# Optimization experiments

Hardware: AMD Instinct MI355X
Metric: run time of the kernel (lower is better)

Reference implementation:

```python
import jax, jax.numpy as jnp
import numpy as np

# Geometry constants matching PointLoss.__init__ defaults
FOV_H = 360.0   # horizontal FOV (deg)
FOV_VU = 3.0    # upper vertical FOV (deg)
DH = 0.5        # delta_h
DV = 0.5        # delta_v
PROJ_H = 52     # int(26 / 0.5)
PROJ_W = 720    # int(360 / 0.5)
THETAC = 0.5    # confidence threshold
LAMDA = 1.0     # fov-loss weight
ANGRATE = 1.0   # anglelossrate
EPS = 1e-8


def setup_inputs() -> dict:
    key = jax.random.key(0)
    ks = jax.random.split(key, 10)
    B, H, W = 64, PROJ_H, PROJ_W
    return {
        "vertexmap_proj": jax.random.normal(ks[0], (B, H, W, 3), jnp.float32),
        "normalmap_proj": jax.random.normal(ks[1], (B, H, W, 3), jnp.float32),
        "uncertainty": jax.random.uniform(ks[2], (B, H, W), jnp.float32),
        "now_normalmap": jax.random.normal(ks[3], (B, H, W, 3), jnp.float32),
        "now_confidencemap": jax.random.uniform(ks[4], (B, H, W), jnp.float32),
        "last_normalmap": jax.random.normal(ks[5], (B, H, W, 3), jnp.float32),
        "last_vertexmap": jax.random.normal(ks[6], (B, H, W, 3), jnp.float32),
        "sx": jnp.zeros((1,), jnp.float32),
        "sq": jnp.zeros((1,), jnp.float32),
        "now_maskmap": jax.random.randint(ks[7], (B, H, W), 0, 2, jnp.int32),
        "last_maskmap": jax.random.randint(ks[8], (B, H, W), 0, 2, jnp.int32),
    }


def _gather_proj(m, flat_idx, B, H, W):
    """Gather pixels of m [B,H,W,(C)] at flat index [B,H,W] -> same shape as m."""
    if m.ndim == 3:
        mf = m.reshape(B, H * W)
        return jnp.take_along_axis(mf, flat_idx.reshape(B, H * W), axis=1).reshape(B, H, W)
    C = m.shape[-1]
    mf = m.reshape(B, H * W, C)
    idx = jnp.broadcast_to(flat_idx.reshape(B, H * W, 1), (B, H * W, C))
    return jnp.take_along_axis(mf, idx, axis=1).reshape(B, H, W, C)


def reference(vertexmap_proj, normalmap_proj, uncertainty, now_normalmap,
              now_confidencemap, last_normalmap, last_vertexmap, sx, sq,
              now_maskmap, last_maskmap):
    B, H, W, _ = vertexmap_proj.shape
    v = vertexmap_proj

    # mask of valid current pixels: maskmap > 0 and normal non-zero
    mask0 = (now_maskmap > 0) & (jnp.sum(jnp.abs(now_normalmap), -1) != 0)

    # spherical re-projection (movegrid=True)
    depth = jnp.sqrt(jnp.sum(v * v, -1) + EPS)
    yaw = jnp.arctan2(v[..., 1], v[..., 0]) * (180.0 / np.pi)
    pitch = jnp.arcsin(jnp.clip(v[..., 2] / depth, -1.0, 1.0)) * (180.0 / np.pi)
    proj_x = (FOV_H / 2 - yaw) / DH
    proj_y = (FOV_VU - pitch) / DV

    # fov loss = masked mse(proj, clamp(proj)) (F.mse_loss default mean)
    m0 = mask0.astype(v.dtype)
    n0 = jnp.maximum(jnp.sum(m0), 1.0)
    fovloss = (jnp.sum(m0 * (proj_x - jnp.clip(proj_x, 0, W - 1)) ** 2)
               + jnp.sum(m0 * (proj_y - jnp.clip(proj_y, 0, H - 1)) ** 2)) / n0

    prx = jnp.round(proj_x)
    pry = jnp.round(proj_y)
    inb = (prx >= 0) & (prx < W) & (pry >= 0) & (pry < H)
    prxi = jnp.clip(prx, 0, W - 1).astype(jnp.int32)
    pryi = jnp.clip(pry, 0, H - 1).astype(jnp.int32)
    flat = pryi * W + prxi  # [B,H,W]

    nl = _gather_proj(last_normalmap, flat, B, H, W)   # last normal at projected pixel
    vl = _gather_proj(last_vertexmap, flat, B, H, W)   # last vertex at projected pixel
    lm = _gather_proj(last_maskmap, flat, B, H, W)

    lastmask = (lm > 0) & (jnp.sum(jnp.abs(nl), -1) != 0)
    mask = mask0 & inb & lastmask & (now_confidencemap >= THETAC)
    m = mask.astype(v.dtype)
    n = jnp.maximum(jnp.sum(m), 1.0)

    # point-to-plane ICP residual, uncertainty-weighted L1
    r = jnp.sum(nl * (v - vl), -1)
    icploss = jnp.sum(m * uncertainty * jnp.abs(r)) / n

    # angular loss: 1 - |cos(angle between normals)|
    nn = normalmap_proj
    cosang = jnp.abs(jnp.sum(nl * nn, -1)) / jnp.sqrt(
        jnp.sum(nl * nl, -1) * jnp.sum(nn * nn, -1) + EPS)
    angloss = jnp.sum(m * uncertainty * (1.0 - cosang)) / n

    sx0, sq0 = sx[0], sq[0]
    total = (jnp.exp(-sx0) * icploss + sx0
             + ANGRATE * jnp.exp(-sq0) * angloss + sq0
             + LAMDA * fovloss)
    return total
```

## Files before the change

### kernel.cpp

```cpp
#include <hip/hip_runtime.h>
#include <math.h>


namespace {
constexpr int B_ = 64, H_ = 52, W_ = 720;
constexpr int HW_ = H_ * W_;
constexpr int NPIX = B_ * HW_;
constexpr int NBLOCKS = 2048;
constexpr int NTHREADS = 256;
constexpr float EPSF = 1e-8f;
constexpr float RAD2DEG = 57.29577951308232f;
}

__global__ __launch_bounds__(NTHREADS) void pointloss_main(
    const float* __restrict__ v,
    const float* __restrict__ nrm,
    const float* __restrict__ unc,
    const float* __restrict__ nown,
    const float* __restrict__ conf,
    const float* __restrict__ lastn,
    const float* __restrict__ lastv,
    const int*   __restrict__ nowm,
    const int*   __restrict__ lastm,
    float* __restrict__ partials)
{
    float s_m0 = 0.f, s_fov = 0.f, s_m = 0.f, s_icp = 0.f, s_ang = 0.f;
    const int stride = NBLOCKS * NTHREADS;
    for (int p = blockIdx.x * NTHREADS + threadIdx.x; p < NPIX; p += stride) {
        const float vx = v[3*p+0], vy = v[3*p+1], vz = v[3*p+2];
        const float ax = nown[3*p+0], ay = nown[3*p+1], az = nown[3*p+2];
        const bool mask0 = (nowm[p] > 0) &&
                           ((fabsf(ax) + fabsf(ay) + fabsf(az)) != 0.0f);

        const float depth = sqrtf(vx*vx + vy*vy + vz*vz + EPSF);
        const float yaw   = atan2f(vy, vx) * RAD2DEG;
        const float pitch = asinf(fminf(fmaxf(vz / depth, -1.f), 1.f)) * RAD2DEG;
        const float px = (180.0f - yaw) * 2.0f;
        const float py = (3.0f - pitch) * 2.0f;

        if (mask0) {
            const float dx = px - fminf(fmaxf(px, 0.f), (float)(W_ - 1));
            const float dy = py - fminf(fmaxf(py, 0.f), (float)(H_ - 1));
            s_m0 += 1.0f;
            s_fov += dx*dx + dy*dy;
        }

        const float prx = rintf(px), pry = rintf(py);
        const bool inb = (prx >= 0.f) && (prx < (float)W_) &&
                         (pry >= 0.f) && (pry < (float)H_);

        if (mask0 && inb && (conf[p] >= 0.5f)) {
            const int gi = (p / HW_) * HW_ + (int)pry * W_ + (int)prx;
            const float lx = lastn[3*gi+0], ly = lastn[3*gi+1], lz = lastn[3*gi+2];
            if ((lastm[gi] > 0) && ((fabsf(lx) + fabsf(ly) + fabsf(lz)) != 0.f)) {
                const float u  = unc[p];
                const float wx = lastv[3*gi+0], wy = lastv[3*gi+1], wz = lastv[3*gi+2];
                const float r  = lx*(vx-wx) + ly*(vy-wy) + lz*(vz-wz);
                const float nx = nrm[3*p+0], ny = nrm[3*p+1], nz = nrm[3*p+2];
                const float dt = lx*nx + ly*ny + lz*nz;
                const float den = (lx*lx + ly*ly + lz*lz) *
                                  (nx*nx + ny*ny + nz*nz) + EPSF;
                const float cosang = fabsf(dt) * rsqrtf(den);
                s_m   += 1.0f;
                s_icp += u * fabsf(r);
                s_ang += u * (1.0f - cosang);
            }
        }
    }

    #pragma unroll
    for (int off = 32; off > 0; off >>= 1) {
        s_m0  += __shfl_down(s_m0,  off);
        s_fov += __shfl_down(s_fov, off);
        s_m   += __shfl_down(s_m,   off);
        s_icp += __shfl_down(s_icp, off);
        s_ang += __shfl_down(s_ang, off);
    }
    __shared__ float red[NTHREADS / 64][5];
    const int lane = threadIdx.x & 63;
    const int wv   = threadIdx.x >> 6;
    if (lane == 0) {
        red[wv][0] = s_m0;  red[wv][1] = s_fov; red[wv][2] = s_m;
        red[wv][3] = s_icp; red[wv][4] = s_ang;
    }
    __syncthreads();
    if (threadIdx.x == 0) {
        float t[5] = {0.f, 0.f, 0.f, 0.f, 0.f};
        for (int w2 = 0; w2 < NTHREADS / 64; ++w2)
            for (int c = 0; c < 5; ++c) t[c] += red[w2][c];
        float* o = partials + blockIdx.x * 5;
        for (int c = 0; c < 5; ++c) o[c] = t[c];
    }
}

__global__ __launch_bounds__(256) void pointloss_finalize(
    const float* __restrict__ partials,
    const float* __restrict__ sx,
    const float* __restrict__ sq,
    float* __restrict__ out)
{
    double a0 = 0, a1 = 0, a2 = 0, a3 = 0, a4 = 0;
    for (int i = threadIdx.x; i < NBLOCKS; i += 256) {
        const float* pp = partials + i * 5;
        a0 += (double)pp[0]; a1 += (double)pp[1]; a2 += (double)pp[2];
        a3 += (double)pp[3]; a4 += (double)pp[4];
    }
    #pragma unroll
    for (int off = 32; off > 0; off >>= 1) {
        a0 += __shfl_down(a0, off);
        a1 += __shfl_down(a1, off);
        a2 += __shfl_down(a2, off);
        a3 += __shfl_down(a3, off);
        a4 += __shfl_down(a4, off);
    }
    __shared__ double red[4][5];
    const int lane = threadIdx.x & 63;
    const int wv   = threadIdx.x >> 6;
    if (lane == 0) {
        red[wv][0] = a0; red[wv][1] = a1; red[wv][2] = a2;
        red[wv][3] = a3; red[wv][4] = a4;
    }
    __syncthreads();
    if (threadIdx.x == 0) {
        double t[5] = {0, 0, 0, 0, 0};
        for (int w2 = 0; w2 < 4; ++w2)
            for (int c = 0; c < 5; ++c) t[c] += red[w2][c];
        const double n0 = fmax(t[0], 1.0);
        const double n  = fmax(t[2], 1.0);
        const double sx0 = (double)sx[0], sq0 = (double)sq[0];
        const double total = exp(-sx0) * (t[3] / n) + sx0
                           + exp(-sq0) * (t[4] / n) + sq0
                           + t[1] / n0;
        out[0] = (float)total;
    }
}

extern "C" void kernel_launch(void* const* d_in, const int* in_sizes, int n_in,
                              void* d_out, int out_size, void* d_ws, size_t ws_size,
                              hipStream_t stream) {
    const float* v     = (const float*)d_in[0];
    const float* nrm   = (const float*)d_in[1];
    const float* unc   = (const float*)d_in[2];
    const float* nown  = (const float*)d_in[3];
    const float* conf  = (const float*)d_in[4];
    const float* lastn = (const float*)d_in[5];
    const float* lastv = (const float*)d_in[6];
    const float* sx    = (const float*)d_in[7];
    const float* sq    = (const float*)d_in[8];
    const int*   nowm  = (const int*)d_in[9];
    const int*   lastm = (const int*)d_in[10];

    float* partials = (float*)d_ws;

    pointloss_main<<<NBLOCKS, NTHREADS, 0, stream>>>(
        v, nrm, unc, nown, conf, lastn, lastv, nowm, lastm, partials);
    pointloss_finalize<<<1, 256, 0, stream>>>(partials, sx, sq, (float*)d_out);
}
```

Measured before the change: 190.6 us.

## Vectorize dense loads per pixel quad and batch gather loads

Each thread now handles fixed quads of four pixels, loading vertex, normal, mask and confidence data with 128-bit vector loads instead of scalar strided loads. The grid is sized to tile the quads exactly, replacing the grid-stride loop. The dependent gathers from the previous frame are issued for all four pixels before any are consumed, to raise memory-level parallelism. This increases register pressure and ties the kernel to the fixed problem size.

```diff
diff --git a/kernel.cpp b/kernel.cpp
--- a/kernel.cpp
+++ b/kernel.cpp
@@ -6,11 +6,16 @@
 constexpr int B_ = 64, H_ = 52, W_ = 720;
 constexpr int HW_ = H_ * W_;
 constexpr int NPIX = B_ * HW_;
-constexpr int NBLOCKS = 2048;
+constexpr int QPI  = HW_ / 4;
+constexpr int NQUAD = NPIX / 4;
 constexpr int NTHREADS = 256;
+constexpr int QPT = 2;
+constexpr int NBLOCKS = NQUAD / (NTHREADS * QPT);
+constexpr int TQUADS = NBLOCKS * NTHREADS;
 constexpr float EPSF = 1e-8f;
 constexpr float RAD2DEG = 57.29577951308232f;
 }
+static_assert(NBLOCKS * NTHREADS * QPT == NQUAD, "grid must tile quads exactly");
 
 __global__ __launch_bounds__(NTHREADS) void pointloss_main(
     const float* __restrict__ v,
@@ -25,45 +30,92 @@
     float* __restrict__ partials)
 {
     float s_m0 = 0.f, s_fov = 0.f, s_m = 0.f, s_icp = 0.f, s_ang = 0.f;
-    const int stride = NBLOCKS * NTHREADS;
-    for (int p = blockIdx.x * NTHREADS + threadIdx.x; p < NPIX; p += stride) {
-        const float vx = v[3*p+0], vy = v[3*p+1], vz = v[3*p+2];
-        const float ax = nown[3*p+0], ay = nown[3*p+1], az = nown[3*p+2];
-        const bool mask0 = (nowm[p] > 0) &&
-                           ((fabsf(ax) + fabsf(ay) + fabsf(az)) != 0.0f);
-
-        const float depth = sqrtf(vx*vx + vy*vy + vz*vz + EPSF);
-        const float yaw   = atan2f(vy, vx) * RAD2DEG;
-        const float pitch = asinf(fminf(fmaxf(vz / depth, -1.f), 1.f)) * RAD2DEG;
-        const float px = (180.0f - yaw) * 2.0f;
-        const float py = (3.0f - pitch) * 2.0f;
-
-        if (mask0) {
-            const float dx = px - fminf(fmaxf(px, 0.f), (float)(W_ - 1));
-            const float dy = py - fminf(fmaxf(py, 0.f), (float)(H_ - 1));
-            s_m0 += 1.0f;
-            s_fov += dx*dx + dy*dy;
+
+    const float4* __restrict__ v4 = (const float4*)v;
+    const float4* __restrict__ n4 = (const float4*)nown;
+    const int4*   __restrict__ m4 = (const int4*)nowm;
+    const float4* __restrict__ c4 = (const float4*)conf;
+
+    const int tid = blockIdx.x * NTHREADS + threadIdx.x;
+
+    #pragma unroll
+    for (int it = 0; it < QPT; ++it) {
+        const int q  = tid + it * TQUADS;
+        const int p0 = q * 4;
+        const int gbase = (q / QPI) * HW_;
+
+        const float4 va = v4[3*q+0], vb = v4[3*q+1], vc = v4[3*q+2];
+        const float4 na = n4[3*q+0], nb = n4[3*q+1], nc = n4[3*q+2];
+        const int4   mm = m4[q];
+        const float4 cf = c4[q];
+
+        const float vx[4] = {va.x, va.w, vb.z, vc.y};
+        const float vy[4] = {va.y, vb.x, vb.w, vc.z};
+        const float vz[4] = {va.z, vb.y, vc.x, vc.w};
+        const float ax[4] = {na.x, na.w, nb.z, nc.y};
+        const float ay[4] = {na.y, nb.x, nb.w, nc.z};
+        const float az[4] = {na.z, nb.y, nc.x, nc.w};
+        const int   mk[4] = {mm.x, mm.y, mm.z, mm.w};
+        const float cv[4] = {cf.x, cf.y, cf.z, cf.w};
+
+        bool g[4];
+        int  gi[4];
+        #pragma unroll
+        for (int j = 0; j < 4; ++j) {
+            const bool mask0 = (mk[j] > 0) &&
+                ((fabsf(ax[j]) + fabsf(ay[j]) + fabsf(az[j])) != 0.0f);
+
+            const float depth = sqrtf(vx[j]*vx[j] + vy[j]*vy[j] + vz[j]*vz[j] + EPSF);
+            const float yaw   = atan2f(vy[j], vx[j]) * RAD2DEG;
+            const float pitch = asinf(fminf(fmaxf(vz[j] / depth, -1.f), 1.f)) * RAD2DEG;
+            const float px = (180.0f - yaw) * 2.0f;
+            const float py = (3.0f - pitch) * 2.0f;
+
+            if (mask0) {
+                const float dx = px - fminf(fmaxf(px, 0.f), (float)(W_ - 1));
+                const float dy = py - fminf(fmaxf(py, 0.f), (float)(H_ - 1));
+                s_m0  += 1.0f;
+                s_fov += dx*dx + dy*dy;
+            }
+
+            const float prx = rintf(px), pry = rintf(py);
+            const bool inb = (prx >= 0.f) && (prx < (float)W_) &&
+                             (pry >= 0.f) && (pry < (float)H_);
+            g[j]  = mask0 && inb && (cv[j] >= 0.5f);
+            gi[j] = g[j] ? (gbase + (int)pry * W_ + (int)prx) : 0;
         }
 
-        const float prx = rintf(px), pry = rintf(py);
-        const bool inb = (prx >= 0.f) && (prx < (float)W_) &&
-                         (pry >= 0.f) && (pry < (float)H_);
-
-        if (mask0 && inb && (conf[p] >= 0.5f)) {
-            const int gi = (p / HW_) * HW_ + (int)pry * W_ + (int)prx;
-            const float lx = lastn[3*gi+0], ly = lastn[3*gi+1], lz = lastn[3*gi+2];
-            if ((lastm[gi] > 0) && ((fabsf(lx) + fabsf(ly) + fabsf(lz)) != 0.f)) {
-                const float u  = unc[p];
-                const float wx = lastv[3*gi+0], wy = lastv[3*gi+1], wz = lastv[3*gi+2];
-                const float r  = lx*(vx-wx) + ly*(vy-wy) + lz*(vz-wz);
-                const float nx = nrm[3*p+0], ny = nrm[3*p+1], nz = nrm[3*p+2];
-                const float dt = lx*nx + ly*ny + lz*nz;
-                const float den = (lx*lx + ly*ly + lz*lz) *
-                                  (nx*nx + ny*ny + nz*nz) + EPSF;
+        float lx[4] = {0,0,0,0}, ly[4] = {0,0,0,0}, lz[4] = {0,0,0,0};
+        float wx[4] = {0,0,0,0}, wy[4] = {0,0,0,0}, wz[4] = {0,0,0,0};
+        float nx[4] = {0,0,0,0}, ny[4] = {0,0,0,0}, nz[4] = {0,0,0,0};
+        float uu[4] = {0,0,0,0};
+        int   lm[4] = {0,0,0,0};
+        #pragma unroll
+        for (int j = 0; j < 4; ++j) {
+            if (g[j]) {
+                const int gi3 = 3 * gi[j];
+                const int p   = p0 + j;
+                lx[j] = lastn[gi3+0]; ly[j] = lastn[gi3+1]; lz[j] = lastn[gi3+2];
+                lm[j] = lastm[gi[j]];
+                wx[j] = lastv[gi3+0]; wy[j] = lastv[gi3+1]; wz[j] = lastv[gi3+2];
+                nx[j] = nrm[3*p+0];   ny[j] = nrm[3*p+1];   nz[j] = nrm[3*p+2];
+                uu[j] = unc[p];
+            }
+        }
+
+        #pragma unroll
+        for (int j = 0; j < 4; ++j) {
+            if (g[j] && (lm[j] > 0) &&
+                ((fabsf(lx[j]) + fabsf(ly[j]) + fabsf(lz[j])) != 0.f)) {
+                const float r  = lx[j]*(vx[j]-wx[j]) + ly[j]*(vy[j]-wy[j])
+                               + lz[j]*(vz[j]-wz[j]);
+                const float dt = lx[j]*nx[j] + ly[j]*ny[j] + lz[j]*nz[j];
+                const float den = (lx[j]*lx[j] + ly[j]*ly[j] + lz[j]*lz[j]) *
+                                  (nx[j]*nx[j] + ny[j]*ny[j] + nz[j]*nz[j]) + EPSF;
                 const float cosang = fabsf(dt) * rsqrtf(den);
                 s_m   += 1.0f;
-                s_icp += u * fabsf(r);
-                s_ang += u * (1.0f - cosang);
+                s_icp += uu[j] * fabsf(r);
+                s_ang += uu[j] * (1.0f - cosang);
             }
         }
     }
```

Result: slower. 197.3 us (+3.5%).
